# Kernel optimization log

Hardware: AMD Instinct MI355X
Metric: run time of the kernel (lower is better)

The kernel has to match this reference:

```python
import jax, jax.numpy as jnp
import numpy as np

N = 30000      # nodes
E = 480000     # edges (before self loops)
C = 64         # in_channels
L = 32         # latent_dim
H = 2          # heads
SLOPE = 0.2    # PyG GATConv default negative_slope


def _param(key, shape, fan_in):
    return jax.random.normal(key, shape, jnp.float32) * (1.0 / np.sqrt(fan_in))


def setup_inputs() -> dict:
    key = jax.random.key(0)
    ks = jax.random.split(key, 32)
    d = {
        "x": jax.random.normal(ks[0], (N, C), jnp.float32),
        "edge_index": jax.random.randint(ks[1], (2, E), 0, N),
        "use_neighbors": 1,
        # GATConv params: W [heads*out, in], att_src/att_dst [heads, out], bias [heads*out]
        # encoder_conv1: in=C, out=2C, heads=H
        "W1": _param(ks[2], (H * 2 * C, C), C),
        "as1": _param(ks[3], (H, 2 * C), 2 * C),
        "ad1": _param(ks[4], (H, 2 * C), 2 * C),
        "b1": jnp.zeros((H * 2 * C,), jnp.float32),
        # encoder_conv2: in=2C*H, out=L, heads=1
        "W2": _param(ks[5], (L, 2 * C * H), 2 * C * H),
        "as2": _param(ks[6], (1, L), L),
        "ad2": _param(ks[7], (1, L), L),
        "b2": jnp.zeros((L,), jnp.float32),
        # decoder_conv1: in=L, out=2C, heads=H
        "W3": _param(ks[8], (H * 2 * C, L), L),
        "as3": _param(ks[9], (H, 2 * C), 2 * C),
        "ad3": _param(ks[10], (H, 2 * C), 2 * C),
        "b3": jnp.zeros((H * 2 * C,), jnp.float32),
        # decoder_conv2: in=2C*H, out=C, heads=1
        "W4": _param(ks[11], (C, 2 * C * H), 2 * C * H),
        "as4": _param(ks[12], (1, C), C),
        "ad4": _param(ks[13], (1, C), C),
        "b4": jnp.zeros((C,), jnp.float32),
        # dense (non-neighbor) branch Linear params [out, in] + bias
        "el1w": _param(ks[14], (2 * C, C), C), "el1b": jnp.zeros((2 * C,), jnp.float32),
        "el2w": _param(ks[15], (L, 2 * C), 2 * C), "el2b": jnp.zeros((L,), jnp.float32),
        "dl1w": _param(ks[16], (2 * C, L), L), "dl1b": jnp.zeros((2 * C,), jnp.float32),
        "dl2w": _param(ks[17], (C, 2 * C), 2 * C), "dl2b": jnp.zeros((C,), jnp.float32),
    }
    return d


def gat_conv(x, src, dst, W, att_src, att_dst, bias, heads, out_ch):
    """PyG GATConv (concat=True, self loops already in src/dst)."""
    n = x.shape[0]
    h = (x @ W.T).reshape(n, heads, out_ch)            # [N,H,F]
    a_s = jnp.sum(h * att_src[None], -1)               # [N,H]
    a_d = jnp.sum(h * att_dst[None], -1)               # [N,H]
    e = jax.nn.leaky_relu(a_s[src] + a_d[dst], SLOPE)  # [Etot,H]
    m = jax.ops.segment_max(e, dst, num_segments=n)
    ex = jnp.exp(e - m[dst])
    den = jax.ops.segment_sum(ex, dst, num_segments=n)
    alpha = ex / den[dst]                              # segment softmax over incoming edges
    msg = h[src] * alpha[..., None]                    # [Etot,H,F]
    out = jax.ops.segment_sum(msg, dst, num_segments=n)
    return out.reshape(n, heads * out_ch) + bias


def reference(x, edge_index, use_neighbors,
              W1, as1, ad1, b1, W2, as2, ad2, b2,
              W3, as3, ad3, b3, W4, as4, ad4, b4,
              el1w, el1b, el2w, el2b, dl1w, dl1b, dl2w, dl2b):
    if use_neighbors:
        loops = jnp.arange(N)
        src = jnp.concatenate([edge_index[0], loops])
        dst = jnp.concatenate([edge_index[1], loops])
        h = jax.nn.relu(gat_conv(x, src, dst, W1, as1, ad1, b1, H, 2 * C))
        z = gat_conv(h, src, dst, W2, as2, ad2, b2, 1, L)
        h = jax.nn.relu(gat_conv(z, src, dst, W3, as3, ad3, b3, H, 2 * C))
        return gat_conv(h, src, dst, W4, as4, ad4, b4, 1, C)
    else:
        h = jax.nn.relu(x @ el1w.T + el1b)
        z = h @ el2w.T + el2b
        h = jax.nn.relu(z @ dl1w.T + dl1b)
        return h @ dl2w.T + dl2b
```

## Files before the change

### kernel.cpp

```cpp
#include <hip/hip_runtime.h>
#include <hip/hip_bf16.h>
#include <math.h>

#define NODES 30000
#define WAVE 64
#define SCAN_T 1024
#define SCAN_CH 32
#define SCAN_CAP (SCAN_T * SCAN_CH)

typedef __attribute__((ext_vector_type(8))) short short8b;
typedef __attribute__((ext_vector_type(4))) float floatx4;

static __device__ __forceinline__ float lrelu(float x) {
    return (x > 0.f) ? x : 0.2f * x;
}

static __device__ __forceinline__ unsigned short f2bf(float f) {
    union { float f; unsigned u; } v; v.f = f;
    unsigned r = v.u + 0x7FFF + ((v.u >> 16) & 1);
    return (unsigned short)(r >> 16);
}

template <int K, int M, int OUT_BF16, int RELU, int DOTS>
__global__ __launch_bounds__(256) void gemm_mfma(
    const unsigned short* __restrict__ Xb, int ldx,
    const unsigned short* __restrict__ Wb,
    const float* __restrict__ bias,
    void* __restrict__ outv, int ldc,
    const float* __restrict__ att_s, const float* __restrict__ att_d,
    float* __restrict__ as_out, float* __restrict__ ad_out,
    const int* __restrict__ flag, int Nrows)
{
    if (*flag == 0) return;
    constexpr int KC = K / 32;
    const int w    = threadIdx.x >> 6;
    const int lane = threadIdx.x & 63;
    const int z    = blockIdx.z;
    const int ct   = blockIdx.y;
    const int rowBase = blockIdx.x * 64 + w * 16;

    const int lr = lane & 15;
    const int lk = (lane >> 4) * 8;

    const int arow = min(rowBase + lr, Nrows - 1);
    const unsigned short* ap = Xb + (size_t)arow * ldx + z * K + lk;
    short8b a[KC];
#pragma unroll
    for (int kc = 0; kc < KC; kc++)
        a[kc] = *reinterpret_cast<const short8b*>(ap + kc * 32);

    const unsigned short* bp = Wb + (size_t)(z * M + ct * 16 + lr) * K + lk;
    short8b b[KC];
#pragma unroll
    for (int kc = 0; kc < KC; kc++)
        b[kc] = *reinterpret_cast<const short8b*>(bp + kc * 32);

    floatx4 c = {0.f, 0.f, 0.f, 0.f};
#pragma unroll
    for (int kc = 0; kc < KC; kc++)
        c = __builtin_amdgcn_mfma_f32_16x16x32_bf16(a[kc], b[kc], c, 0, 0, 0);

    const int colg = z * M + ct * 16 + lr;
    const float bv = bias ? bias[colg] : 0.f;

#pragma unroll
    for (int i = 0; i < 4; i++) {
        int r = rowBase + (lane >> 4) * 4 + i;
        float v = c[i] + bv;
        if (RELU) v = fmaxf(v, 0.f);
        if (r < Nrows) {
            if (OUT_BF16)
                ((unsigned short*)outv)[(size_t)r * ldc + colg] = f2bf(v);
            else
                ((float*)outv)[(size_t)r * ldc + colg] = v;
        }
    }

    if (DOTS) {
        const float as_v = att_s[colg];
        const float ad_v = att_d[colg];
#pragma unroll
        for (int i = 0; i < 4; i++) {
            int r = rowBase + (lane >> 4) * 4 + i;
            float ps = c[i] * as_v;
            float pd = c[i] * ad_v;
#pragma unroll
            for (int off = 8; off; off >>= 1) {
                ps += __shfl_xor(ps, off);
                pd += __shfl_xor(pd, off);
            }
            if (lr == 0 && r < Nrows) {
                atomicAdd(&as_out[r], ps);
                atomicAdd(&ad_out[r], pd);
            }
        }
    }
}

__global__ __launch_bounds__(256) void gemm_xwt(
    const float* __restrict__ X, int lda, const float* __restrict__ W,
    const float* __restrict__ bias, float* __restrict__ out, int ldc,
    int Nrows, int M, int K, int relu,
    const int* __restrict__ flag, int wantFlag)
{
    if (((*flag != 0) ? 1 : 0) != wantFlag) return;

    const int z = blockIdx.z;
    X += (size_t)z * K;
    W += (size_t)z * M * K;
    if (bias) bias += (size_t)z * M;
    out += (size_t)z * M;

    __shared__ float As[16][68];
    __shared__ float Bs[16][68];

    const int t  = threadIdx.x;
    const int tx = t & 15;
    const int ty = t >> 4;
    const int rowBase = blockIdx.y * 64;
    const int colBase = blockIdx.x * 64;

    float acc[4][4];
#pragma unroll
    for (int i = 0; i < 4; i++)
#pragma unroll
        for (int j = 0; j < 4; j++) acc[i][j] = 0.f;

    const int r_ld = t >> 2;
    const int k_ld = (t & 3) * 4;

    for (int kt = 0; kt < K; kt += 16) {
        float4 av = make_float4(0.f, 0.f, 0.f, 0.f);
        int grow = rowBase + r_ld;
        if (grow < Nrows)
            av = *reinterpret_cast<const float4*>(&X[(size_t)grow * lda + kt + k_ld]);
        As[k_ld + 0][r_ld] = av.x;
        As[k_ld + 1][r_ld] = av.y;
        As[k_ld + 2][r_ld] = av.z;
        As[k_ld + 3][r_ld] = av.w;
        float4 bv = make_float4(0.f, 0.f, 0.f, 0.f);
        int gm = colBase + r_ld;
        if (gm < M)
            bv = *reinterpret_cast<const float4*>(&W[(size_t)gm * K + kt + k_ld]);
        Bs[k_ld + 0][r_ld] = bv.x;
        Bs[k_ld + 1][r_ld] = bv.y;
        Bs[k_ld + 2][r_ld] = bv.z;
        Bs[k_ld + 3][r_ld] = bv.w;
        __syncthreads();

#pragma unroll
        for (int kk = 0; kk < 16; ++kk) {
            const float4 a = *reinterpret_cast<const float4*>(&As[kk][ty * 4]);
            const float4 b = *reinterpret_cast<const float4*>(&Bs[kk][tx * 4]);
            acc[0][0] += a.x * b.x; acc[0][1] += a.x * b.y; acc[0][2] += a.x * b.z; acc[0][3] += a.x * b.w;
            acc[1][0] += a.y * b.x; acc[1][1] += a.y * b.y; acc[1][2] += a.y * b.z; acc[1][3] += a.y * b.w;
            acc[2][0] += a.z * b.x; acc[2][1] += a.z * b.y; acc[2][2] += a.z * b.z; acc[2][3] += a.z * b.w;
            acc[3][0] += a.w * b.x; acc[3][1] += a.w * b.y; acc[3][2] += a.w * b.z; acc[3][3] += a.w * b.w;
        }
        __syncthreads();
    }

#pragma unroll
    for (int i = 0; i < 4; i++) {
        int row = rowBase + ty * 4 + i;
        if (row >= Nrows) continue;
        int col0 = colBase + tx * 4;
        if (col0 >= M) continue;
        float4 v = make_float4(acc[i][0], acc[i][1], acc[i][2], acc[i][3]);
        if (bias) {
            v.x += bias[col0 + 0]; v.y += bias[col0 + 1];
            v.z += bias[col0 + 2]; v.w += bias[col0 + 3];
        }
        if (relu) {
            v.x = fmaxf(v.x, 0.f); v.y = fmaxf(v.y, 0.f);
            v.z = fmaxf(v.z, 0.f); v.w = fmaxf(v.w, 0.f);
        }
        *reinterpret_cast<float4*>(&out[(size_t)row * ldc + col0]) = v;
    }
}

__global__ void cvt_bf16(const float* __restrict__ s0, unsigned short* __restrict__ d0, int n0,
                         const float* __restrict__ s1, unsigned short* __restrict__ d1, int n1,
                         const float* __restrict__ s2, unsigned short* __restrict__ d2, int n2,
                         const float* __restrict__ s3, unsigned short* __restrict__ d3, int n3,
                         const int* __restrict__ flag)
{
    if (*flag == 0) return;
    int i = blockIdx.x * blockDim.x + threadIdx.x;
    if (i < n0) { d0[i] = f2bf(s0[i]); return; }
    i -= n0;
    if (i < n1) { d1[i] = f2bf(s1[i]); return; }
    i -= n1;
    if (i < n2) { d2[i] = f2bf(s2[i]); return; }
    i -= n2;
    if (i < n3) d3[i] = f2bf(s3[i]);
}

__global__ void zero_f2(float* __restrict__ a, float* __restrict__ b, int n,
                        const int* __restrict__ flag)
{
    if (*flag == 0) return;
    int i = blockIdx.x * blockDim.x + threadIdx.x;
    if (i < n) { a[i] = 0.f; b[i] = 0.f; }
}

template <int HH, int F, int K>
__global__ __launch_bounds__(256) void fold_att(
    const float* __restrict__ W, const float* __restrict__ as_,
    const float* __restrict__ ad_, float* __restrict__ us,
    float* __restrict__ ud, const int* __restrict__ flag)
{
    if (*flag == 0) return;
    const int b   = blockIdx.x;
    const int sel = b / HH;
    const int h   = b % HH;
    const float* att = sel ? ad_ : as_;
    float* uo = sel ? ud : us;

    constexpr int NG = 256 / K;
    const int k  = threadIdx.x % K;
    const int fg = threadIdx.x / K;

    float s = 0.f;
#pragma unroll
    for (int f = fg; f < F; f += NG)
        s += att[h * F + f] * W[(size_t)(h * F + f) * K + k];

    __shared__ float red[256];
    red[threadIdx.x] = s;
    __syncthreads();
    if (fg == 0) {
        float tot = s;
#pragma unroll
        for (int g = 1; g < NG; g++) tot += red[g * K + k];
        uo[h * K + k] = tot;
    }
}

template <int K, int HH>
__global__ __launch_bounds__(256) void att_from_x(
    const float* __restrict__ xin, const float* __restrict__ us,
    const float* __restrict__ ud, float* __restrict__ as_out,
    float* __restrict__ ad_out, const int* __restrict__ flag)
{
    if (*flag == 0) return;
    constexpr int NPW = WAVE / K;
    const int wid  = threadIdx.x >> 6;
    const int lane = threadIdx.x & 63;
    const int sub  = lane / K;
    const int col  = lane % K;
    const int node = (blockIdx.x * 4 + wid) * NPW + sub;

    float v = 0.f;
    if (node < NODES) v = xin[(size_t)node * K + col];
    float ps[HH], pd[HH];
#pragma unroll
    for (int h = 0; h < HH; h++) {
        ps[h] = v * us[h * K + col];
        pd[h] = v * ud[h * K + col];
    }
#pragma unroll
    for (int off = K / 2; off; off >>= 1) {
#pragma unroll
        for (int h = 0; h < HH; h++) {
            ps[h] += __shfl_xor(ps[h], off);
            pd[h] += __shfl_xor(pd[h], off);
        }
    }
    if (col == 0 && node < NODES) {
#pragma unroll
        for (int h = 0; h < HH; h++) {
            as_out[node * HH + h] = ps[h];
            ad_out[node * HH + h] = pd[h];
        }
    }
}

template <int K, int HH>
__global__ __launch_bounds__(256) void gat_aggr_x(
    const float* __restrict__ xin, const float* __restrict__ as_,
    const float* __restrict__ ad_, const int* __restrict__ rowptr,
    const int* __restrict__ csr_src, unsigned short* __restrict__ aggb,
    const int* __restrict__ flag)
{
    if (*flag == 0) return;
    const int node = blockIdx.x * 4 + (threadIdx.x >> 6);
    const int lane = threadIdx.x & 63;
    if (node >= NODES) return;

    const int beg = rowptr[node], end = rowptr[node + 1];
    const int deg = end - beg;

    float adv[HH];
#pragma unroll
    for (int h = 0; h < HH; h++) adv[h] = ad_[node * HH + h];

    float wl[HH];
    float mx[HH], rden[HH];
    const bool fast = (deg <= WAVE);

    if (fast) {
        float e[HH];
        int i = beg + lane;
        if (i < end) {
            int s = csr_src[i];
#pragma unroll
            for (int h = 0; h < HH; h++)
                e[h] = lrelu(as_[s * HH + h] + adv[h]);
        } else {
#pragma unroll
            for (int h = 0; h < HH; h++) e[h] = -1e30f;
        }
#pragma unroll
        for (int h = 0; h < HH; h++) {
            mx[h] = e[h];
#pragma unroll
            for (int off = 32; off; off >>= 1)
                mx[h] = fmaxf(mx[h], __shfl_xor(mx[h], off));
            float ex = __expf(e[h] - mx[h]);
            wl[h] = ex;
            float dn = ex;
#pragma unroll
            for (int off = 32; off; off >>= 1)
                dn += __shfl_xor(dn, off);
            rden[h] = 1.f / dn;
        }
    } else {
        float den[HH];
#pragma unroll
        for (int h = 0; h < HH; h++) { mx[h] = -1e30f; den[h] = 0.f; }
        for (int i = beg + lane; i < end; i += WAVE) {
            int s = csr_src[i];
#pragma unroll
            for (int h = 0; h < HH; h++)
                mx[h] = fmaxf(mx[h], lrelu(as_[s * HH + h] + adv[h]));
        }
#pragma unroll
        for (int h = 0; h < HH; h++)
#pragma unroll
            for (int off = 32; off; off >>= 1)
                mx[h] = fmaxf(mx[h], __shfl_xor(mx[h], off));
        for (int i = beg + lane; i < end; i += WAVE) {
            int s = csr_src[i];
#pragma unroll
            for (int h = 0; h < HH; h++)
                den[h] += __expf(lrelu(as_[s * HH + h] + adv[h]) - mx[h]);
        }
#pragma unroll
        for (int h = 0; h < HH; h++) {
#pragma unroll
            for (int off = 32; off; off >>= 1)
                den[h] += __shfl_xor(den[h], off);
            rden[h] = 1.f / den[h];
        }
    }

    constexpr int LPG = K / 4;
    constexpr int GR  = WAVE / LPG;
    const int esub = lane / LPG;
    const int c4   = lane % LPG;

    float4 acc[HH];
#pragma unroll
    for (int h = 0; h < HH; h++) acc[h] = make_float4(0.f, 0.f, 0.f, 0.f);

    if (fast) {
        const int iters = (deg + GR - 1) / GR;
        for (int it = 0; it < iters; ++it) {
            const int i = beg + it * GR + esub;
            const bool valid = (i < end);
            const int srcl = valid ? (i - beg) : 0;
            float w[HH];
#pragma unroll
            for (int h = 0; h < HH; h++)
                w[h] = __shfl(wl[h], srcl);
            if (valid) {
                int s = csr_src[i];
                float4 xv = *reinterpret_cast<const float4*>(&xin[(size_t)s * K + c4 * 4]);
#pragma unroll
                for (int h = 0; h < HH; h++) {
                    acc[h].x += xv.x * w[h];
                    acc[h].y += xv.y * w[h];
                    acc[h].z += xv.z * w[h];
                    acc[h].w += xv.w * w[h];
                }
            }
        }
    } else {
        for (int i = beg + esub; i < end; i += GR) {
            int s = csr_src[i];
            float w[HH];
#pragma unroll
            for (int h = 0; h < HH; h++)
                w[h] = __expf(lrelu(as_[s * HH + h] + adv[h]) - mx[h]);
            float4 xv = *reinterpret_cast<const float4*>(&xin[(size_t)s * K + c4 * 4]);
#pragma unroll
            for (int h = 0; h < HH; h++) {
                acc[h].x += xv.x * w[h];
                acc[h].y += xv.y * w[h];
                acc[h].z += xv.z * w[h];
                acc[h].w += xv.w * w[h];
            }
        }
    }
#pragma unroll
    for (int off = LPG; off < WAVE; off <<= 1) {
#pragma unroll
        for (int h = 0; h < HH; h++) {
            acc[h].x += __shfl_xor(acc[h].x, off);
            acc[h].y += __shfl_xor(acc[h].y, off);
            acc[h].z += __shfl_xor(acc[h].z, off);
            acc[h].w += __shfl_xor(acc[h].w, off);
        }
    }
    if (esub == 0) {
#pragma unroll
        for (int h = 0; h < HH; h++) {
            ushort4 o;
            o.x = f2bf(acc[h].x * rden[h]);
            o.y = f2bf(acc[h].y * rden[h]);
            o.z = f2bf(acc[h].z * rden[h]);
            o.w = f2bf(acc[h].w * rden[h]);
            *reinterpret_cast<ushort4*>(&aggb[(size_t)node * (HH * K) + h * K + c4 * 4]) = o;
        }
    }
}

template <int HF, int RELU>
__global__ __launch_bounds__(256) void gat_aggr_h(
    const float* __restrict__ hsrc, const float* __restrict__ as_,
    const float* __restrict__ ad_, const int* __restrict__ rowptr,
    const int* __restrict__ csr_src, const float* __restrict__ bias,
    float* __restrict__ out, const int* __restrict__ flag)
{
    if (*flag == 0) return;
    const int node = blockIdx.x * 4 + (threadIdx.x >> 6);
    const int lane = threadIdx.x & 63;
    if (node >= NODES) return;

    const int beg = rowptr[node], end = rowptr[node + 1];
    const int deg = end - beg;
    const float adv = ad_[node];

    float wl, mx, rden;
    const bool fast = (deg <= WAVE);

    if (fast) {
        int i = beg + lane;
        float e = -1e30f;
        if (i < end) {
            int s = csr_src[i];
            e = lrelu(as_[s] + adv);
        }
        mx = e;
#pragma unroll
        for (int off = 32; off; off >>= 1)
            mx = fmaxf(mx, __shfl_xor(mx, off));
        wl = __expf(e - mx);
        float dn = wl;
#pragma unroll
        for (int off = 32; off; off >>= 1)
            dn += __shfl_xor(dn, off);
        rden = 1.f / dn;
    } else {
        mx = -1e30f;
        float den = 0.f;
        for (int i = beg + lane; i < end; i += WAVE) {
            int s = csr_src[i];
            mx = fmaxf(mx, lrelu(as_[s] + adv));
        }
#pragma unroll
        for (int off = 32; off; off >>= 1)
            mx = fmaxf(mx, __shfl_xor(mx, off));
        for (int i = beg + lane; i < end; i += WAVE) {
            int s = csr_src[i];
            den += __expf(lrelu(as_[s] + adv) - mx);
        }
#pragma unroll
        for (int off = 32; off; off >>= 1)
            den += __shfl_xor(den, off);
        rden = 1.f / den;
        wl = 0.f;
    }

    constexpr int LPG = HF / 4;
    constexpr int GR  = WAVE / LPG;
    const int esub = lane / LPG;
    const int c4   = lane % LPG;

    float4 acc = make_float4(0.f, 0.f, 0.f, 0.f);
    if (fast) {
        const int iters = (deg + GR - 1) / GR;
        for (int it = 0; it < iters; ++it) {
            const int i = beg + it * GR + esub;
            const bool valid = (i < end);
            const int srcl = valid ? (i - beg) : 0;
            float w = __shfl(wl, srcl);
            if (valid) {
                int s = csr_src[i];
                float4 hv = *reinterpret_cast<const float4*>(&hsrc[(size_t)s * HF + c4 * 4]);
                acc.x += hv.x * w; acc.y += hv.y * w; acc.z += hv.z * w; acc.w += hv.w * w;
            }
        }
    } else {
        for (int i = beg + esub; i < end; i += GR) {
            int s = csr_src[i];
            float w = __expf(lrelu(as_[s] + adv) - mx);
            float4 hv = *reinterpret_cast<const float4*>(&hsrc[(size_t)s * HF + c4 * 4]);
            acc.x += hv.x * w; acc.y += hv.y * w; acc.z += hv.z * w; acc.w += hv.w * w;
        }
    }
#pragma unroll
    for (int off = LPG; off < WAVE; off <<= 1) {
        acc.x += __shfl_xor(acc.x, off);
        acc.y += __shfl_xor(acc.y, off);
        acc.z += __shfl_xor(acc.z, off);
        acc.w += __shfl_xor(acc.w, off);
    }
    if (esub == 0) {
        float4 bv = *reinterpret_cast<const float4*>(&bias[c4 * 4]);
        float4 o = make_float4(acc.x * rden + bv.x, acc.y * rden + bv.y,
                               acc.z * rden + bv.z, acc.w * rden + bv.w);
        if (RELU) {
            o.x = fmaxf(o.x, 0.f); o.y = fmaxf(o.y, 0.f);
            o.z = fmaxf(o.z, 0.f); o.w = fmaxf(o.w, 0.f);
        }
        *reinterpret_cast<float4*>(&out[(size_t)node * HF + c4 * 4]) = o;
    }
}

__global__ void zero_int(int* __restrict__ p, int n, const int* __restrict__ flag)
{
    if (*flag == 0) return;
    for (int i = blockIdx.x * blockDim.x + threadIdx.x; i < n; i += gridDim.x * blockDim.x)
        p[i] = 0;
}

__global__ void count_deg(const int* __restrict__ ei, int* __restrict__ deg,
                          int E_, int Nn, const int* __restrict__ flag)
{
    if (*flag == 0) return;
    int e = blockIdx.x * blockDim.x + threadIdx.x;
    int tot = E_ + Nn;
    if (e >= tot) return;
    int dst = (e < E_) ? ei[E_ + e] : (e - E_);
    atomicAdd(&deg[dst], 1);
}

__global__ __launch_bounds__(SCAN_T) void scan_deg(
    const int* __restrict__ deg, int* __restrict__ rowptr,
    int* __restrict__ cursor, const int* __restrict__ flag)
{
    if (*flag == 0) return;
    __shared__ int sums[SCAN_T];
    const int t = threadIdx.x;
    const int base = t * SCAN_CH;

    int v[SCAN_CH];
    const int4* dp = reinterpret_cast<const int4*>(deg + base);
#pragma unroll
    for (int j = 0; j < SCAN_CH / 4; j++) {
        int4 q = dp[j];
        v[4 * j + 0] = q.x; v[4 * j + 1] = q.y;
        v[4 * j + 2] = q.z; v[4 * j + 3] = q.w;
    }
    int s = 0;
#pragma unroll
    for (int j = 0; j < SCAN_CH; j++) s += v[j];
    sums[t] = s;
    __syncthreads();
    for (int off = 1; off < SCAN_T; off <<= 1) {
        int x = (t >= off) ? sums[t - off] : 0;
        __syncthreads();
        sums[t] += x;
        __syncthreads();
    }
    int run = sums[t] - s;
    if (t == 0) rowptr[0] = 0;
#pragma unroll
    for (int j = 0; j < SCAN_CH; j++) {
        cursor[base + j] = run;
        run += v[j];
        rowptr[base + j + 1] = run;
    }
}

__global__ void scatter_edges(const int* __restrict__ ei, int* __restrict__ cursor,
                              int* __restrict__ csr_src, int E_, int Nn,
                              const int* __restrict__ flag)
{
    if (*flag == 0) return;
    int e = blockIdx.x * blockDim.x + threadIdx.x;
    int tot = E_ + Nn;
    if (e >= tot) return;
    int src, dst;
    if (e < E_) { src = ei[e]; dst = ei[E_ + e]; }
    else        { src = e - E_; dst = src; }
    int pos = atomicAdd(&cursor[dst], 1);
    csr_src[pos] = src;
}

extern "C" void kernel_launch(void* const* d_in, const int* in_sizes, int n_in,
                              void* d_out, int out_size, void* d_ws, size_t ws_size,
                              hipStream_t stream)
{
    const float* x    = (const float*)d_in[0];
    const int*   ei   = (const int*)d_in[1];
    const int*   flag = (const int*)d_in[2];
    const float* W1 = (const float*)d_in[3];
    const float* as1 = (const float*)d_in[4];
    const float* ad1 = (const float*)d_in[5];
    const float* b1 = (const float*)d_in[6];
    const float* W2 = (const float*)d_in[7];
    const float* as2 = (const float*)d_in[8];
    const float* ad2 = (const float*)d_in[9];
    const float* b2 = (const float*)d_in[10];
    const float* W3 = (const float*)d_in[11];
    const float* as3 = (const float*)d_in[12];
    const float* ad3 = (const float*)d_in[13];
    const float* b3 = (const float*)d_in[14];
    const float* W4 = (const float*)d_in[15];
    const float* as4 = (const float*)d_in[16];
    const float* ad4 = (const float*)d_in[17];
    const float* b4 = (const float*)d_in[18];
    const float* el1w = (const float*)d_in[19];
    const float* el1b = (const float*)d_in[20];
    const float* el2w = (const float*)d_in[21];
    const float* el2b = (const float*)d_in[22];
    const float* dl1w = (const float*)d_in[23];
    const float* dl1b = (const float*)d_in[24];
    const float* dl2w = (const float*)d_in[25];
    const float* dl2b = (const float*)d_in[26];

    const int E_   = in_sizes[1] / 2;
    const int Etot = E_ + NODES;

    char* base = (char*)d_ws;
    size_t off = 0;
    auto carve = [&](size_t bytes) -> void* {
        void* p = base + off;
        off = (off + bytes + 255) & ~(size_t)255;
        return p;
    };
    float* T0  = (float*)carve((size_t)NODES * 128 * 4);
    float* A   = (float*)carve((size_t)NODES * 256 * 4);
    float* T1  = (float*)carve((size_t)NODES * 64 * 4);
    float* Bz  = (float*)carve((size_t)NODES * 32 * 4);
    float* asb = (float*)carve((size_t)NODES * 2 * 4);
    float* adb = (float*)carve((size_t)NODES * 2 * 4);
    float* u1s = (float*)carve(2 * 64 * 4);
    float* u1d = (float*)carve(2 * 64 * 4);
    float* u3s = (float*)carve(2 * 32 * 4);
    float* u3d = (float*)carve(2 * 32 * 4);
    unsigned short* aggb = (unsigned short*)carve((size_t)NODES * 128 * 2);
    unsigned short* Ab   = (unsigned short*)carve((size_t)NODES * 256 * 2);
    unsigned short* wb1  = (unsigned short*)carve(256 * 64 * 2);
    unsigned short* wb2  = (unsigned short*)carve(32 * 256 * 2);
    unsigned short* wb3  = (unsigned short*)carve(256 * 32 * 2);
    unsigned short* wb4  = (unsigned short*)carve(64 * 256 * 2);
    int* deg    = (int*)carve((size_t)SCAN_CAP * 4);
    int* rowptr = (int*)carve((size_t)(SCAN_CAP + 1) * 4);
    int* cursor = (int*)carve((size_t)SCAN_CAP * 4);
    int* csr    = (int*)carve((size_t)Etot * 4);
    (void)ws_size; (void)n_in; (void)out_size;

    float* outp = (float*)d_out;

    const int nodeBlocks = (NODES + 3) / 4;
    const int edgeBlocks = (Etot + 255) / 256;
    dim3 blk(256);
    const int rowTiles = (NODES + 63) / 64;

    zero_int<<<(SCAN_CAP + 255) / 256, 256, 0, stream>>>(deg, SCAN_CAP, flag);
    count_deg<<<edgeBlocks, 256, 0, stream>>>(ei, deg, E_, NODES, flag);
    scan_deg<<<1, SCAN_T, 0, stream>>>(deg, rowptr, cursor, flag);
    scatter_edges<<<edgeBlocks, 256, 0, stream>>>(ei, cursor, csr, E_, NODES, flag);
    cvt_bf16<<<(16384 + 8192 + 8192 + 16384 + 255) / 256, 256, 0, stream>>>(
        W1, wb1, 16384, W2, wb2, 8192, W3, wb3, 8192, W4, wb4, 16384, flag);

    fold_att<2, 128, 64><<<4, 256, 0, stream>>>(W1, as1, ad1, u1s, u1d, flag);
    att_from_x<64, 2><<<nodeBlocks, blk, 0, stream>>>(x, u1s, u1d, asb, adb, flag);
    gat_aggr_x<64, 2><<<nodeBlocks, blk, 0, stream>>>(x, asb, adb, rowptr, csr, aggb, flag);
    gemm_mfma<64, 128, 1, 1, 0><<<dim3(rowTiles, 8, 2), blk, 0, stream>>>(
        aggb, 128, wb1, b1, Ab, 256, nullptr, nullptr, nullptr, nullptr, flag, NODES);

    zero_f2<<<(NODES + 255) / 256, 256, 0, stream>>>(asb, adb, NODES, flag);
    gemm_mfma<256, 32, 0, 0, 1><<<dim3(rowTiles, 2, 1), blk, 0, stream>>>(
        Ab, 256, wb2, nullptr, T1, 32, as2, ad2, asb, adb, flag, NODES);
    gat_aggr_h<32, 0><<<nodeBlocks, blk, 0, stream>>>(T1, asb, adb, rowptr, csr, b2, Bz, flag);

    fold_att<2, 128, 32><<<4, 256, 0, stream>>>(W3, as3, ad3, u3s, u3d, flag);
    att_from_x<32, 2><<<(NODES + 7) / 8, blk, 0, stream>>>(Bz, u3s, u3d, asb, adb, flag);
    gat_aggr_x<32, 2><<<nodeBlocks, blk, 0, stream>>>(Bz, asb, adb, rowptr, csr, aggb, flag);
    gemm_mfma<32, 128, 1, 1, 0><<<dim3(rowTiles, 8, 2), blk, 0, stream>>>(
        aggb, 64, wb3, b3, Ab, 256, nullptr, nullptr, nullptr, nullptr, flag, NODES);

    zero_f2<<<(NODES + 255) / 256, 256, 0, stream>>>(asb, adb, NODES, flag);
    gemm_mfma<256, 64, 0, 0, 1><<<dim3(rowTiles, 4, 1), blk, 0, stream>>>(
        Ab, 256, wb4, nullptr, T1, 64, as4, ad4, asb, adb, flag, NODES);
    gat_aggr_h<64, 0><<<nodeBlocks, blk, 0, stream>>>(T1, asb, adb, rowptr, csr, b4, outp, flag);

    gemm_xwt<<<dim3(2, rowTiles, 1), blk, 0, stream>>>(x,  64,  el1w, el1b, T0,   128, NODES, 128, 64, 1, flag, 0);
    gemm_xwt<<<dim3(1, rowTiles, 1), blk, 0, stream>>>(T0, 128, el2w, el2b, Bz,   32,  NODES, 32, 128, 0, flag, 0);
    gemm_xwt<<<dim3(2, rowTiles, 1), blk, 0, stream>>>(Bz, 32,  dl1w, dl1b, A,    128, NODES, 128, 32, 1, flag, 0);
    gemm_xwt<<<dim3(1, rowTiles, 1), blk, 0, stream>>>(A,  128, dl2w, dl2b, outp, 64,  NODES, 64, 128, 0, flag, 0);
}
```

Measured before the change: 383.9 us.

## Gather bf16 features in GAT aggregation and merge prep kernels

Every neighbor-gather in the GAT aggregation kernels now reads node features as bf16: x is converted once up front, and the layer-2 output is also written as bf16. The GEMMs feeding the attention aggregation emit bf16 directly. The zero, weight-convert and degree-clear kernels are folded into a single grid-stride prep kernel, with dedicated attention buffers so the mid-pipeline zeroing launches go away. The goal is to halve gather bandwidth and cut launches, at the cost of bf16 rounding on the aggregated features.

```diff
diff --git a/kernel.cpp b/kernel.cpp
--- a/kernel.cpp
+++ b/kernel.cpp
@@ -19,6 +19,53 @@
     union { float f; unsigned u; } v; v.f = f;
     unsigned r = v.u + 0x7FFF + ((v.u >> 16) & 1);
     return (unsigned short)(r >> 16);
+}
+
+static __device__ __forceinline__ void unpack8(uint4 q, float* v) {
+    v[0] = __uint_as_float(q.x << 16); v[1] = __uint_as_float(q.x & 0xFFFF0000u);
+    v[2] = __uint_as_float(q.y << 16); v[3] = __uint_as_float(q.y & 0xFFFF0000u);
+    v[4] = __uint_as_float(q.z << 16); v[5] = __uint_as_float(q.z & 0xFFFF0000u);
+    v[6] = __uint_as_float(q.w << 16); v[7] = __uint_as_float(q.w & 0xFFFF0000u);
+}
+
+static __device__ __forceinline__ uint4 pack8(const float* v) {
+    uint4 p;
+    p.x = (unsigned)f2bf(v[0]) | ((unsigned)f2bf(v[1]) << 16);
+    p.y = (unsigned)f2bf(v[2]) | ((unsigned)f2bf(v[3]) << 16);
+    p.z = (unsigned)f2bf(v[4]) | ((unsigned)f2bf(v[5]) << 16);
+    p.w = (unsigned)f2bf(v[6]) | ((unsigned)f2bf(v[7]) << 16);
+    return p;
+}
+
+__global__ __launch_bounds__(256) void prep(
+    int* __restrict__ deg,
+    float* __restrict__ z0, float* __restrict__ z1,
+    float* __restrict__ z2, float* __restrict__ z3,
+    const float* __restrict__ W1, unsigned short* __restrict__ wb1,
+    const float* __restrict__ W2, unsigned short* __restrict__ wb2,
+    const float* __restrict__ W3, unsigned short* __restrict__ wb3,
+    const float* __restrict__ W4, unsigned short* __restrict__ wb4,
+    const float* __restrict__ x, unsigned short* __restrict__ xb,
+    const int* __restrict__ flag)
+{
+    if (*flag == 0) return;
+    const int tid = blockIdx.x * blockDim.x + threadIdx.x;
+    const int stride = gridDim.x * blockDim.x;
+    for (int i = tid; i < SCAN_CAP / 4; i += stride)
+        reinterpret_cast<int4*>(deg)[i] = make_int4(0, 0, 0, 0);
+    for (int i = tid; i < NODES; i += stride) {
+        z0[i] = 0.f; z1[i] = 0.f; z2[i] = 0.f; z3[i] = 0.f;
+    }
+    for (int i = tid; i < 256 * 64; i += stride) wb1[i] = f2bf(W1[i]);
+    for (int i = tid; i < 32 * 256; i += stride) wb2[i] = f2bf(W2[i]);
+    for (int i = tid; i < 256 * 32; i += stride) wb3[i] = f2bf(W3[i]);
+    for (int i = tid; i < 64 * 256; i += stride) wb4[i] = f2bf(W4[i]);
+    for (int i = tid; i < NODES * 64 / 4; i += stride) {
+        float4 v = reinterpret_cast<const float4*>(x)[i];
+        ushort4 o;
+        o.x = f2bf(v.x); o.y = f2bf(v.y); o.z = f2bf(v.z); o.w = f2bf(v.w);
+        reinterpret_cast<ushort4*>(xb)[i] = o;
+    }
 }
 
 template <int K, int M, int OUT_BF16, int RELU, int DOTS>
@@ -179,31 +226,6 @@
     }
 }
 
-__global__ void cvt_bf16(const float* __restrict__ s0, unsigned short* __restrict__ d0, int n0,
-                         const float* __restrict__ s1, unsigned short* __restrict__ d1, int n1,
-                         const float* __restrict__ s2, unsigned short* __restrict__ d2, int n2,
-                         const float* __restrict__ s3, unsigned short* __restrict__ d3, int n3,
-                         const int* __restrict__ flag)
-{
-    if (*flag == 0) return;
-    int i = blockIdx.x * blockDim.x + threadIdx.x;
-    if (i < n0) { d0[i] = f2bf(s0[i]); return; }
-    i -= n0;
-    if (i < n1) { d1[i] = f2bf(s1[i]); return; }
-    i -= n1;
-    if (i < n2) { d2[i] = f2bf(s2[i]); return; }
-    i -= n2;
-    if (i < n3) d3[i] = f2bf(s3[i]);
-}
-
-__global__ void zero_f2(float* __restrict__ a, float* __restrict__ b, int n,
-                        const int* __restrict__ flag)
-{
-    if (*flag == 0) return;
-    int i = blockIdx.x * blockDim.x + threadIdx.x;
-    if (i < n) { a[i] = 0.f; b[i] = 0.f; }
-}
-
 template <int HH, int F, int K>
 __global__ __launch_bounds__(256) void fold_att(
     const float* __restrict__ W, const float* __restrict__ as_,
@@ -278,7 +300,7 @@
 
 template <int K, int HH>
 __global__ __launch_bounds__(256) void gat_aggr_x(
-    const float* __restrict__ xin, const float* __restrict__ as_,
+    const unsigned short* __restrict__ xb, const float* __restrict__ as_,
     const float* __restrict__ ad_, const int* __restrict__ rowptr,
     const int* __restrict__ csr_src, unsigned short* __restrict__ aggb,
     const int* __restrict__ flag)
@@ -353,16 +375,19 @@
                 den[h] += __shfl_xor(den[h], off);
             rden[h] = 1.f / den[h];
         }
-    }
-
-    constexpr int LPG = K / 4;
+        wl[0] = 0.f;
+    }
+
+    constexpr int LPG = K / 8;
     constexpr int GR  = WAVE / LPG;
     const int esub = lane / LPG;
-    const int c4   = lane % LPG;
-
-    float4 acc[HH];
-#pragma unroll
-    for (int h = 0; h < HH; h++) acc[h] = make_float4(0.f, 0.f, 0.f, 0.f);
+    const int c8   = lane % LPG;
+
+    float acc[HH][8];
+#pragma unroll
+    for (int h = 0; h < HH; h++)
+#pragma unroll
+        for (int j = 0; j < 8; j++) acc[h][j] = 0.f;
 
     if (fast) {
         const int iters = (deg + GR - 1) / GR;
@@ -376,14 +401,14 @@
                 w[h] = __shfl(wl[h], srcl);
             if (valid) {
                 int s = csr_src[i];
-                float4 xv = *reinterpret_cast<const float4*>(&xin[(size_t)s * K + c4 * 4]);
-#pragma unroll
-                for (int h = 0; h < HH; h++) {
-                    acc[h].x += xv.x * w[h];
-                    acc[h].y += xv.y * w[h];
-                    acc[h].z += xv.z * w[h];
-                    acc[h].w += xv.w * w[h];
-                }
+                uint4 q = *reinterpret_cast<const uint4*>(&xb[(size_t)s * K + c8 * 8]);
+                float v[8];
+                unpack8(q, v);
+#pragma unroll
+                for (int h = 0; h < HH; h++)
+#pragma unroll
+                    for (int j = 0; j < 8; j++)
+                        acc[h][j] += v[j] * w[h];
             }
         }
     } else {
@@ -393,45 +418,42 @@
 #pragma unroll
             for (int h = 0; h < HH; h++)
                 w[h] = __expf(lrelu(as_[s * HH + h] + adv[h]) - mx[h]);
-            float4 xv = *reinterpret_cast<const float4*>(&xin[(size_t)s * K + c4 * 4]);
-#pragma unroll
-            for (int h = 0; h < HH; h++) {
-                acc[h].x += xv.x * w[h];
-                acc[h].y += xv.y * w[h];
-                acc[h].z += xv.z * w[h];
-                acc[h].w += xv.w * w[h];
-            }
-        }
-    }
-#pragma unroll
-    for (int off = LPG; off < WAVE; off <<= 1) {
+            uint4 q = *reinterpret_cast<const uint4*>(&xb[(size_t)s * K + c8 * 8]);
+            float v[8];
+            unpack8(q, v);
+#pragma unroll
+            for (int h = 0; h < HH; h++)
+#pragma unroll
+                for (int j = 0; j < 8; j++)
+                    acc[h][j] += v[j] * w[h];
+        }
+    }
+#pragma unroll
+    for (int off = LPG; off < WAVE; off <<= 1)
+#pragma unroll
+        for (int h = 0; h < HH; h++)
+#pragma unroll
+            for (int j = 0; j < 8; j++)
+                acc[h][j] += __shfl_xor(acc[h][j], off);
+
+    if (esub == 0) {
 #pragma unroll
         for (int h = 0; h < HH; h++) {
-            acc[h].x += __shfl_xor(acc[h].x, off);
-            acc[h].y += __shfl_xor(acc[h].y, off);
-            acc[h].z += __shfl_xor(acc[h].z, off);
-            acc[h].w += __shfl_xor(acc[h].w, off);
-        }
-    }
-    if (esub == 0) {
-#pragma unroll
-        for (int h = 0; h < HH; h++) {
-            ushort4 o;
-            o.x = f2bf(acc[h].x * rden[h]);
-            o.y = f2bf(acc[h].y * rden[h]);
-            o.z = f2bf(acc[h].z * rden[h]);
-            o.w = f2bf(acc[h].w * rden[h]);
-            *reinterpret_cast<ushort4*>(&aggb[(size_t)node * (HH * K) + h * K + c4 * 4]) = o;
-        }
-    }
-}
-
-template <int HF, int RELU>
+            float o[8];
+#pragma unroll
+            for (int j = 0; j < 8; j++) o[j] = acc[h][j] * rden[h];
+            *reinterpret_cast<uint4*>(&aggb[(size_t)node * (HH * K) + h * K + c8 * 8]) = pack8(o);
+        }
+    }
+}
+
+template <int HF, int RELU, int OUTB>
 __global__ __launch_bounds__(256) void gat_aggr_h(
-    const float* __restrict__ hsrc, const float* __restrict__ as_,
+    const unsigned short* __restrict__ hb, const float* __restrict__ as_,
     const float* __restrict__ ad_, const int* __restrict__ rowptr,
     const int* __restrict__ csr_src, const float* __restrict__ bias,
-    float* __restrict__ out, const int* __restrict__ flag)
+    float* __restrict__ out, unsigned short* __restrict__ outb,
+    const int* __restrict__ flag)
 {
     if (*flag == 0) return;
     const int node = blockIdx.x * 4 + (threadIdx.x >> 6);
@@ -483,12 +505,15 @@
         wl = 0.f;
     }
 
-    constexpr int LPG = HF / 4;
+    constexpr int LPG = HF / 8;
     constexpr int GR  = WAVE / LPG;
     const int esub = lane / LPG;
-    const int c4   = lane % LPG;
-
-    float4 acc = make_float4(0.f, 0.f, 0.f, 0.f);
+    const int c8   = lane % LPG;
+
+    float acc[8];
+#pragma unroll
+    for (int j = 0; j < 8; j++) acc[j] = 0.f;
+
     if (fast) {
         const int iters = (deg + GR - 1) / GR;
         for (int it = 0; it < iters; ++it) {
@@ -498,42 +523,45 @@
             float w = __shfl(wl, srcl);
             if (valid) {
                 int s = csr_src[i];
-                float4 hv = *reinterpret_cast<const float4*>(&hsrc[(size_t)s * HF + c4 * 4]);
-                acc.x += hv.x * w; acc.y += hv.y * w; acc.z += hv.z * w; acc.w += hv.w * w;
+                uint4 q = *reinterpret_cast<const uint4*>(&hb[(size_t)s * HF + c8 * 8]);
+                float v[8];
+                unpack8(q, v);
+#pragma unroll
+                for (int j = 0; j < 8; j++) acc[j] += v[j] * w;
             }
         }
     } else {
         for (int i = beg + esub; i < end; i += GR) {
             int s = csr_src[i];
             float w = __expf(lrelu(as_[s] + adv) - mx);
-            float4 hv = *reinterpret_cast<const float4*>(&hsrc[(size_t)s * HF + c4 * 4]);
-            acc.x += hv.x * w; acc.y += hv.y * w; acc.z += hv.z * w; acc.w += hv.w * w;
-        }
-    }
-#pragma unroll
-    for (int off = LPG; off < WAVE; off <<= 1) {
-        acc.x += __shfl_xor(acc.x, off);
-        acc.y += __shfl_xor(acc.y, off);
-        acc.z += __shfl_xor(acc.z, off);
-        acc.w += __shfl_xor(acc.w, off);
-    }
+            uint4 q = *reinterpret_cast<const uint4*>(&hb[(size_t)s * HF + c8 * 8]);
+            float v[8];
+            unpack8(q, v);
+#pragma unroll
+            for (int j = 0; j < 8; j++) acc[j] += v[j] * w;
+        }
+    }
+#pragma unroll
+    for (int off = LPG; off < WAVE; off <<= 1)
+#pragma unroll
+        for (int j = 0; j < 8; j++)
+            acc[j] += __shfl_xor(acc[j], off);
+
     if (esub == 0) {
-        float4 bv = *reinterpret_cast<const float4*>(&bias[c4 * 4]);
-        float4 o = make_float4(acc.x * rden + bv.x, acc.y * rden + bv.y,
-                               acc.z * rden + bv.z, acc.w * rden + bv.w);
-        if (RELU) {
-            o.x = fmaxf(o.x, 0.f); o.y = fmaxf(o.y, 0.f);
-            o.z = fmaxf(o.z, 0.f); o.w = fmaxf(o.w, 0.f);
-        }
-        *reinterpret_cast<float4*>(&out[(size_t)node * HF + c4 * 4]) = o;
-    }
-}
-
-__global__ void zero_int(int* __restrict__ p, int n, const int* __restrict__ flag)
-{
-    if (*flag == 0) return;
-    for (int i = blockIdx.x * blockDim.x + threadIdx.x; i < n; i += gridDim.x * blockDim.x)
-        p[i] = 0;
+        const int col0 = c8 * 8;
+        float o[8];
+#pragma unroll
+        for (int j = 0; j < 8; j++) {
+            o[j] = acc[j] * rden + bias[col0 + j];
+            if (RELU) o[j] = fmaxf(o[j], 0.f);
+        }
+        float4 o0 = make_float4(o[0], o[1], o[2], o[3]);
+        float4 o1 = make_float4(o[4], o[5], o[6], o[7]);
+        *reinterpret_cast<float4*>(&out[(size_t)node * HF + col0]) = o0;
+        *reinterpret_cast<float4*>(&out[(size_t)node * HF + col0 + 4]) = o1;
+        if (OUTB)
+            *reinterpret_cast<uint4*>(&outb[(size_t)node * HF + col0]) = pack8(o);
+    }
 }
 
 __global__ void count_deg(const int* __restrict__ ei, int* __restrict__ deg,
@@ -644,16 +672,22 @@
     };
     float* T0  = (float*)carve((size_t)NODES * 128 * 4);
     float* A   = (float*)carve((size_t)NODES * 256 * 4);
-    float* T1  = (float*)carve((size_t)NODES * 64 * 4);
     float* Bz  = (float*)carve((size_t)NODES * 32 * 4);
     float* asb = (float*)carve((size_t)NODES * 2 * 4);
     float* adb = (float*)carve((size_t)NODES * 2 * 4);
+    float* as2b = (float*)carve((size_t)NODES * 4);
+    float* ad2b = (float*)carve((size_t)NODES * 4);
+    float* as4b = (float*)carve((size_t)NODES * 4);
+    float* ad4b = (float*)carve((size_t)NODES * 4);
     float* u1s = (float*)carve(2 * 64 * 4);
     float* u1d = (float*)carve(2 * 64 * 4);
     float* u3s = (float*)carve(2 * 32 * 4);
     float* u3d = (float*)carve(2 * 32 * 4);
+    unsigned short* xb   = (unsigned short*)carve((size_t)NODES * 64 * 2);
     unsigned short* aggb = (unsigned short*)carve((size_t)NODES * 128 * 2);
     unsigned short* Ab   = (unsigned short*)carve((size_t)NODES * 256 * 2);
+    unsigned short* T1b  = (unsigned short*)carve((size_t)NODES * 64 * 2);
+    unsigned short* Bzb  = (unsigned short*)carve((size_t)NODES * 32 * 2);
     unsigned short* wb1  = (unsigned short*)carve(256 * 64 * 2);
     unsigned short* wb2  = (unsigned short*)carve(32 * 256 * 2);
     unsigned short* wb3  = (unsigned short*)carve(256 * 32 * 2);
@@ -671,34 +705,32 @@
     dim3 blk(256);
     const int rowTiles = (NODES + 63) / 64;
 
-    zero_int<<<(SCAN_CAP + 255) / 256, 256, 0, stream>>>(deg, SCAN_CAP, flag);
+    prep<<<2048, 256, 0, stream>>>(deg, as2b, ad2b, as4b, ad4b,
+                                   W1, wb1, W2, wb2, W3, wb3, W4, wb4,
+                                   x, xb, flag);
     count_deg<<<edgeBlocks, 256, 0, stream>>>(ei, deg, E_, NODES, flag);
     scan_deg<<<1, SCAN_T, 0, stream>>>(deg, rowptr, cursor, flag);
     scatter_edges<<<edgeBlocks, 256, 0, stream>>>(ei, cursor, csr, E_, NODES, flag);
-    cvt_bf16<<<(16384 + 8192 + 8192 + 16384 + 255) / 256, 256, 0, stream>>>(
-        W1, wb1, 16384, W2, wb2, 8192, W3, wb3, 8192, W4, wb4, 16384, flag);
 
     fold_att<2, 128, 64><<<4, 256, 0, stream>>>(W1, as1, ad1, u1s, u1d, flag);
     att_from_x<64, 2><<<nodeBlocks, blk, 0, stream>>>(x, u1s, u1d, asb, adb, flag);
-    gat_aggr_x<64, 2><<<nodeBlocks, blk, 0, stream>>>(x, asb, adb, rowptr, csr, aggb, flag);
+    gat_aggr_x<64, 2><<<nodeBlocks, blk, 0, stream>>>(xb, asb, adb, rowptr, csr, aggb, flag);
     gemm_mfma<64, 128, 1, 1, 0><<<dim3(rowTiles, 8, 2), blk, 0, stream>>>(
         aggb, 128, wb1, b1, Ab, 256, nullptr, nullptr, nullptr, nullptr, flag, NODES);
 
-    zero_f2<<<(NODES + 255) / 256, 256, 0, stream>>>(asb, adb, NODES, flag);
-    gemm_mfma<256, 32, 0, 0, 1><<<dim3(rowTiles, 2, 1), blk, 0, stream>>>(
-        Ab, 256, wb2, nullptr, T1, 32, as2, ad2, asb, adb, flag, NODES);
-    gat_aggr_h<32, 0><<<nodeBlocks, blk, 0, stream>>>(T1, asb, adb, rowptr, csr, b2, Bz, flag);
+    gemm_mfma<256, 32, 1, 0, 1><<<dim3(rowTiles, 2, 1), blk, 0, stream>>>(
+        Ab, 256, wb2, nullptr, T1b, 32, as2, ad2, as2b, ad2b, flag, NODES);
+    gat_aggr_h<32, 0, 1><<<nodeBlocks, blk, 0, stream>>>(T1b, as2b, ad2b, rowptr, csr, b2, Bz, Bzb, flag);
 
     fold_att<2, 128, 32><<<4, 256, 0, stream>>>(W3, as3, ad3, u3s, u3d, flag);
     att_from_x<32, 2><<<(NODES + 7) / 8, blk, 0, stream>>>(Bz, u3s, u3d, asb, adb, flag);
-    gat_aggr_x<32, 2><<<nodeBlocks, blk, 0, stream>>>(Bz, asb, adb, rowptr, csr, aggb, flag);
+    gat_aggr_x<32, 2><<<nodeBlocks, blk, 0, stream>>>(Bzb, asb, adb, rowptr, csr, aggb, flag);
     gemm_mfma<32, 128, 1, 1, 0><<<dim3(rowTiles, 8, 2), blk, 0, stream>>>(
         aggb, 64, wb3, b3, Ab, 256, nullptr, nullptr, nullptr, nullptr, flag, NODES);
 
-    zero_f2<<<(NODES + 255) / 256, 256, 0, stream>>>(asb, adb, NODES, flag);
-    gemm_mfma<256, 64, 0, 0, 1><<<dim3(rowTiles, 4, 1), blk, 0, stream>>>(
-        Ab, 256, wb4, nullptr, T1, 64, as4, ad4, asb, adb, flag, NODES);
-    gat_aggr_h<64, 0><<<nodeBlocks, blk, 0, stream>>>(T1, asb, adb, rowptr, csr, b4, outp, flag);
+    gemm_mfma<256, 64, 1, 0, 1><<<dim3(rowTiles, 4, 1), blk, 0, stream>>>(
+        Ab, 256, wb4, nullptr, T1b, 64, as4, ad4, as4b, ad4b, flag, NODES);
+    gat_aggr_h<64, 0, 0><<<nodeBlocks, blk, 0, stream>>>(T1b, as4b, ad4b, rowptr, csr, b4, outp, nullptr, flag);
 
     gemm_xwt<<<dim3(2, rowTiles, 1), blk, 0, stream>>>(x,  64,  el1w, el1b, T0,   128, NODES, 128, 64, 1, flag, 0);
     gemm_xwt<<<dim3(1, rowTiles, 1), blk, 0, stream>>>(T0, 128, el2w, el2b, Bz,   32,  NODES, 32, 128, 0, flag, 0);
```

Measured after the change: 386.6 us. Within noise of the previous version (+0.7%).
